# Kernel tuning notes

Hardware: AMD Instinct MI355X
Metric: run time of the kernel (lower is better)

Reference implementation:

```python
import jax, jax.numpy as jnp
import numpy as np

B, S, D = 4, 2048, 1024

def setup_inputs() -> dict:
    key = jax.random.key(0)
    ks = jax.random.split(key, 9)
    sc = 1.0 / np.sqrt(D)
    return {
        "x": jax.random.normal(ks[0], (B, S, D), dtype=jnp.float32),
        "Wq": jax.random.normal(ks[1], (D, D), dtype=jnp.float32) * sc,
        "bq": jnp.zeros((D,), dtype=jnp.float32),
        "Wk": jax.random.normal(ks[2], (D, D), dtype=jnp.float32) * sc,
        "bk": jnp.zeros((D,), dtype=jnp.float32),
        "Wv": jax.random.normal(ks[3], (D, D), dtype=jnp.float32) * sc,
        "bv": jnp.zeros((D,), dtype=jnp.float32),
        "Wo": jax.random.normal(ks[4], (D, D), dtype=jnp.float32) * sc,
        "bo": jnp.zeros((D,), dtype=jnp.float32),
    }

def _gaussian_mask(seq_len, dtype):
    # exp(-0.5*((pos - S/2)/(S/4))^2), shape [1,1,S] -> broadcasts over KEY axis
    pos = jnp.arange(seq_len, dtype=dtype)
    center = seq_len / 2
    sigma = seq_len / 4
    m = jnp.exp(-0.5 * ((pos - center) / sigma) ** 2)
    return m[None, None, :]

def reference(x, Wq, bq, Wk, bk, Wv, bv, Wo, bo):
    d = x.shape[-1]
    Q = x @ Wq.T + bq            # [B,S,D]
    K = x @ Wk.T + bk
    V = x @ Wv.T + bv
    scores = jnp.einsum('bqd,bkd->bqk', Q, K) / jnp.sqrt(jnp.asarray(d, x.dtype))
    scores = scores * _gaussian_mask(x.shape[1], x.dtype)
    attn = jax.nn.softmax(scores, axis=-1)
    out = jnp.einsum('bqk,bkd->bqd', attn, V)
    return out @ Wo.T + bo
```

## Files before the change

kernel.cpp:

```cpp
#include <hip/hip_runtime.h>
#include <math.h>

#define SEQ 2048
#define DIM 1024

typedef __attribute__((ext_vector_type(8))) _Float16 half8;
typedef __attribute__((ext_vector_type(4))) float f32x4;

__device__ __forceinline__ unsigned short f2h(float f) {
    union { _Float16 h; unsigned short u; } c; c.h = (_Float16)f;
    return c.u;
}
__device__ __forceinline__ float gmask(int k) {
    float t = ((float)k - 1024.0f) * (1.0f / 512.0f);
    return expf(-0.5f * t * t);
}
__device__ __forceinline__ void glds16(const unsigned short* gp, unsigned short* lp) {
    __builtin_amdgcn_global_load_lds((const __attribute__((address_space(1))) void*)gp,
                                     (__attribute__((address_space(3))) void*)lp, 16, 0, 0);
}

__device__ __forceinline__ void stage64(const unsigned short* __restrict__ g, int ldK,
                                        unsigned short* lds, int wave, int lane) {
    int row = wave * 32 + (lane >> 3);
    int seg = (lane & 7) ^ (lane >> 3);
    const unsigned short* gp = g + (long)row * ldK + seg * 8;
    unsigned short* lp = lds + wave * 2048;
    glds16(gp, lp);
    glds16(gp + 8 * (long)ldK, lp + 512);
    glds16(gp + 16 * (long)ldK, lp + 1024);
    glds16(gp + 24 * (long)ldK, lp + 1536);
}

enum { EPI_QK = 0, EPI_VT = 1, EPI_EXP = 2, EPI_PV = 3, EPI_OUT = 4 };

template <int EPI>
__device__ __forceinline__ void gemm_body(
    const unsigned short* __restrict__ A, const unsigned short* __restrict__ Bm,
    const float* __restrict__ bias,
    float* __restrict__ Cf, unsigned short* __restrict__ Ch,
    int M, int N, int K, float scale, long sA, long sB, long sC)
{
    __shared__ unsigned short As[128 * 64];
    __shared__ unsigned short Bs[128 * 64];

    const int bz = blockIdx.z;
    const int tid = threadIdx.x;
    const int wave = tid >> 6;
    const int lane = tid & 63;
    const int wm = (wave & 1) * 64;
    const int wn = (wave >> 1) * 64;
    const long m0 = (long)blockIdx.y * 128;
    const long n0 = (long)blockIdx.x * 128;
    const int lm = lane & 15;
    const int lk = lane >> 4;

    const unsigned short* pA = A + bz * sA + m0 * K;
    const unsigned short* pB = Bm + bz * sB + n0 * K;

    f32x4 acc[4][4];
#pragma unroll
    for (int i = 0; i < 4; ++i)
#pragma unroll
        for (int j = 0; j < 4; ++j) {
            acc[i][j].x = 0.f; acc[i][j].y = 0.f; acc[i][j].z = 0.f; acc[i][j].w = 0.f;
        }

    int aoff[4][2], boff[4][2];
#pragma unroll
    for (int i = 0; i < 4; ++i)
#pragma unroll
        for (int t = 0; t < 2; ++t) {
            int ar = wm + i * 16 + lm;
            aoff[i][t] = ar * 64 + (((4 * t + lk) ^ (ar & 7)) << 3);
            int br = wn + i * 16 + lm;
            boff[i][t] = br * 64 + (((4 * t + lk) ^ (br & 7)) << 3);
        }

    const int pr = (wave & 1) * 64 + lane;
    const int ph = wave >> 1;
    float psum = 0.f;

    for (int k0 = 0; k0 < K; k0 += 64) {
        stage64(pA + k0, K, As, wave, lane);
        stage64(pB + k0, K, Bs, wave, lane);
        __syncthreads();

        if (EPI == EPI_PV) {
            const unsigned short* rowp = As + pr * 64;
#pragma unroll
            for (int i2 = 0; i2 < 4; ++i2) {
                half8 h = *(const half8*)(rowp + (((2 * i2 + ph) ^ (pr & 7)) << 3));
#pragma unroll
                for (int e = 0; e < 8; ++e) psum += (float)h[e];
            }
        }

#pragma unroll
        for (int t = 0; t < 2; ++t) {
            half8 a[4], b[4];
#pragma unroll
            for (int i = 0; i < 4; ++i) a[i] = *(const half8*)(As + aoff[i][t]);
#pragma unroll
            for (int j = 0; j < 4; ++j) b[j] = *(const half8*)(Bs + boff[j][t]);
#pragma unroll
            for (int i = 0; i < 4; ++i)
#pragma unroll
                for (int j = 0; j < 4; ++j)
                    acc[i][j] = __builtin_amdgcn_mfma_f32_16x16x32_f16(a[i], b[j], acc[i][j], 0, 0, 0);
        }
        __syncthreads();
    }

    float* rsf = (float*)As;
    if (EPI == EPI_PV) {
        rsf[ph * 128 + pr] = psum;
        __syncthreads();
    }

    const long MD = 8388608;
    float* cF = (EPI == EPI_OUT) ? Cf + bz * sC : (float*)nullptr;
    unsigned short* cH = (EPI != EPI_OUT) ? Ch + bz * sC : (unsigned short*)nullptr;

#pragma unroll
    for (int i = 0; i < 4; ++i) {
        long mrow = m0 + wm + i * 16 + lk * 4;
        int lr = wm + i * 16 + lk * 4;
        float inv4[4];
        if (EPI == EPI_PV) {
#pragma unroll
            for (int r = 0; r < 4; ++r)
                inv4[r] = 1.0f / (rsf[lr + r] + rsf[128 + lr + r]);
        }
#pragma unroll
        for (int j = 0; j < 4; ++j) {
            int n = (int)n0 + wn + j * 16 + lm;
            if (EPI == EPI_QK) {
                int sel = n >> 10;
                int n1 = n & 1023;
                float bs = bias[n];
                unsigned short* dst = cH + (long)sel * MD;
#pragma unroll
                for (int r = 0; r < 4; ++r)
                    dst[(mrow + r) * (long)DIM + n1] = f2h(acc[i][j][r] + bs);
            } else if (EPI == EPI_VT) {
                float bs = bias[n];
                long b = mrow >> 11, s = mrow & 2047;
                long idx = 2 * MD + b * (long)DIM * SEQ + (long)n * SEQ + s;
                unsigned long long pk =
                    (unsigned long long)f2h(acc[i][j].x + bs) |
                    ((unsigned long long)f2h(acc[i][j].y + bs) << 16) |
                    ((unsigned long long)f2h(acc[i][j].z + bs) << 32) |
                    ((unsigned long long)f2h(acc[i][j].w + bs) << 48);
                *(unsigned long long*)(cH + idx) = pk;
            } else if (EPI == EPI_EXP) {
                float mult = scale * gmask(n);
#pragma unroll
                for (int r = 0; r < 4; ++r)
                    cH[(mrow + r) * (long)N + n] = f2h(expf(acc[i][j][r] * mult));
            } else if (EPI == EPI_PV) {
#pragma unroll
                for (int r = 0; r < 4; ++r)
                    cH[(mrow + r) * (long)N + n] = f2h(acc[i][j][r] * inv4[r]);
            } else {
                float bs = bias[n];
#pragma unroll
                for (int r = 0; r < 4; ++r)
                    cF[(mrow + r) * (long)N + n] = acc[i][j][r] + bs;
            }
        }
    }
}

__global__ __launch_bounds__(256, 4) void gemm_qk(
    const unsigned short* __restrict__ A, const unsigned short* __restrict__ Bm,
    const float* __restrict__ bias, float* __restrict__ Cf, unsigned short* __restrict__ Ch,
    int M, int N, int K, float scale, long sA, long sB, long sC)
{ gemm_body<EPI_QK>(A, Bm, bias, Cf, Ch, M, N, K, scale, sA, sB, sC); }

__global__ __launch_bounds__(256, 4) void gemm_v(
    const unsigned short* __restrict__ A, const unsigned short* __restrict__ Bm,
    const float* __restrict__ bias, float* __restrict__ Cf, unsigned short* __restrict__ Ch,
    int M, int N, int K, float scale, long sA, long sB, long sC)
{ gemm_body<EPI_VT>(A, Bm, bias, Cf, Ch, M, N, K, scale, sA, sB, sC); }

__global__ __launch_bounds__(256, 4) void gemm_exp(
    const unsigned short* __restrict__ A, const unsigned short* __restrict__ Bm,
    const float* __restrict__ bias, float* __restrict__ Cf, unsigned short* __restrict__ Ch,
    int M, int N, int K, float scale, long sA, long sB, long sC)
{ gemm_body<EPI_EXP>(A, Bm, bias, Cf, Ch, M, N, K, scale, sA, sB, sC); }

__global__ __launch_bounds__(256, 4) void gemm_pv(
    const unsigned short* __restrict__ A, const unsigned short* __restrict__ Bm,
    const float* __restrict__ bias, float* __restrict__ Cf, unsigned short* __restrict__ Ch,
    int M, int N, int K, float scale, long sA, long sB, long sC)
{ gemm_body<EPI_PV>(A, Bm, bias, Cf, Ch, M, N, K, scale, sA, sB, sC); }

__global__ __launch_bounds__(256, 4) void gemm_out(
    const unsigned short* __restrict__ A, const unsigned short* __restrict__ Bm,
    const float* __restrict__ bias, float* __restrict__ Cf, unsigned short* __restrict__ Ch,
    int M, int N, int K, float scale, long sA, long sB, long sC)
{ gemm_body<EPI_OUT>(A, Bm, bias, Cf, Ch, M, N, K, scale, sA, sB, sC); }

__global__ __launch_bounds__(256) void prep(
    const float* __restrict__ x,
    const float* __restrict__ Wq, const float* __restrict__ Wk,
    const float* __restrict__ Wv, const float* __restrict__ Wo,
    const float* __restrict__ b0, const float* __restrict__ b1, const float* __restrict__ b2,
    unsigned short* __restrict__ xh, unsigned short* __restrict__ Wp, float* __restrict__ bqkv)
{
    long gid = (long)blockIdx.x * 256 + threadIdx.x;
    if (gid < 3072) {
        int sel = (int)(gid >> 10);
        const float* s = sel == 0 ? b0 : sel == 1 ? b1 : b2;
        bqkv[gid] = s[gid & 1023];
    }
    const long NX = 8388608 / 4;
    const long NW = 1048576 / 4;
    const long total = NX + 4 * NW;
    for (long i = gid; i < total; i += (long)gridDim.x * 256) {
        const float* src; unsigned short* dst; long off;
        if (i < NX) { src = x; dst = xh; off = i; }
        else {
            long wi = i - NX;
            int sel = (int)(wi >> 18);
            src = sel == 0 ? Wq : sel == 1 ? Wk : sel == 2 ? Wv : Wo;
            dst = Wp + ((long)sel << 20);
            off = wi & (NW - 1);
        }
        float4 v = ((const float4*)src)[off];
        unsigned long long p = (unsigned long long)f2h(v.x) | ((unsigned long long)f2h(v.y) << 16) |
                               ((unsigned long long)f2h(v.z) << 32) | ((unsigned long long)f2h(v.w) << 48);
        ((unsigned long long*)dst)[off] = p;
    }
}

extern "C" void kernel_launch(void* const* d_in, const int* in_sizes, int n_in,
                              void* d_out, int out_size, void* d_ws, size_t ws_size,
                              hipStream_t stream)
{
    const float* x  = (const float*)d_in[0];
    const float* Wq = (const float*)d_in[1];
    const float* bq = (const float*)d_in[2];
    const float* Wk = (const float*)d_in[3];
    const float* bk = (const float*)d_in[4];
    const float* Wv = (const float*)d_in[5];
    const float* bv = (const float*)d_in[6];
    const float* Wo = (const float*)d_in[7];
    const float* bo = (const float*)d_in[8];
    float* out = (float*)d_out;

    const long MD = 4L * SEQ * DIM;
    const long WW = (long)DIM * DIM;
    const long SD = (long)SEQ * DIM, SS = (long)SEQ * SEQ;

    unsigned short* xh   = (unsigned short*)d_ws;
    unsigned short* Wp   = xh + MD;
    unsigned short* Woh  = Wp + 3 * WW;
    float* bqkv          = (float*)(Wp + 4 * WW);
    unsigned short* Qh   = (unsigned short*)(bqkv + 4096);
    unsigned short* VT   = Qh + 2 * MD;
    unsigned short* expS = Qh + 3 * MD;
    unsigned short* O1   = xh;

    dim3 blk(256);
    prep<<<4096, blk, 0, stream>>>(x, Wq, Wk, Wv, Wo, bq, bk, bv, xh, Wp, bqkv);

    gemm_qk<<<dim3(2 * DIM / 128, (4 * SEQ) / 128, 1), blk, 0, stream>>>(
        xh, Wp, bqkv, nullptr, Qh, 4 * SEQ, 2 * DIM, DIM, 1.0f, 0, 0, 0);
    gemm_v<<<dim3(DIM / 128, (4 * SEQ) / 128, 1), blk, 0, stream>>>(
        xh, Wp + 2 * WW, bqkv + 2048, nullptr, Qh, 4 * SEQ, DIM, DIM, 1.0f, 0, 0, 0);
    gemm_exp<<<dim3(SEQ / 128, SEQ / 128, 4), blk, 0, stream>>>(
        Qh, Qh + MD, nullptr, nullptr, expS, SEQ, SEQ, DIM, 0.03125f, SD, SD, SS);
    gemm_pv<<<dim3(DIM / 128, SEQ / 128, 4), blk, 0, stream>>>(
        expS, VT, nullptr, nullptr, O1, SEQ, DIM, SEQ, 1.0f, SS, (long)DIM * SEQ, SD);
    gemm_out<<<dim3(DIM / 128, (4 * SEQ) / 128, 1), blk, 0, stream>>>(
        O1, Woh, bo, out, nullptr, 4 * SEQ, DIM, DIM, 1.0f, 0, 0, 0);
}
```

Baseline: 293.9 us.

## Compute PV row sums with MFMA against ones and remap block indices

In the PV stage, the per-row softmax denominator was accumulated with scalar LDS reads and adds, then reduced through shared memory. It is now computed as an extra MFMA of each A fragment against a vector of ones, so the sum lands in registers aligned with the accumulator rows and the LDS reduction and its barrier go away. Separately, the linear workgroup id is remapped in strides of eight so consecutive blocks are spread across the grid, likely to balance L2 or XCD locality. The ones-MFMA adds 4 extra MFMAs per k-step for every wave of the PV kernel.

```diff
diff --git a/kernel.cpp b/kernel.cpp
--- a/kernel.cpp
+++ b/kernel.cpp
@@ -44,14 +44,21 @@
     __shared__ unsigned short As[128 * 64];
     __shared__ unsigned short Bs[128 * 64];
 
-    const int bz = blockIdx.z;
+    unsigned p = blockIdx.x + gridDim.x * (blockIdx.y + gridDim.y * blockIdx.z);
+    unsigned nwg = gridDim.x * gridDim.y * gridDim.z;
+    unsigned lw = (p & 7) * (nwg >> 3) + (p >> 3);
+    const int bx = lw % gridDim.x;
+    unsigned r1 = lw / gridDim.x;
+    const int by = r1 % gridDim.y;
+    const int bz = r1 / gridDim.y;
+
     const int tid = threadIdx.x;
     const int wave = tid >> 6;
     const int lane = tid & 63;
     const int wm = (wave & 1) * 64;
     const int wn = (wave >> 1) * 64;
-    const long m0 = (long)blockIdx.y * 128;
-    const long n0 = (long)blockIdx.x * 128;
+    const long m0 = (long)by * 128;
+    const long n0 = (long)bx * 128;
     const int lm = lane & 15;
     const int lk = lane >> 4;
 
@@ -65,6 +72,12 @@
         for (int j = 0; j < 4; ++j) {
             acc[i][j].x = 0.f; acc[i][j].y = 0.f; acc[i][j].z = 0.f; acc[i][j].w = 0.f;
         }
+    f32x4 rs[4];
+#pragma unroll
+    for (int i = 0; i < 4; ++i) { rs[i].x = 0.f; rs[i].y = 0.f; rs[i].z = 0.f; rs[i].w = 0.f; }
+    half8 vone;
+#pragma unroll
+    for (int e = 0; e < 8; ++e) vone[e] = (_Float16)1.0f;
 
     int aoff[4][2], boff[4][2];
 #pragma unroll
@@ -77,25 +90,11 @@
             boff[i][t] = br * 64 + (((4 * t + lk) ^ (br & 7)) << 3);
         }
 
-    const int pr = (wave & 1) * 64 + lane;
-    const int ph = wave >> 1;
-    float psum = 0.f;
-
     for (int k0 = 0; k0 < K; k0 += 64) {
         stage64(pA + k0, K, As, wave, lane);
         stage64(pB + k0, K, Bs, wave, lane);
         __syncthreads();
 
-        if (EPI == EPI_PV) {
-            const unsigned short* rowp = As + pr * 64;
-#pragma unroll
-            for (int i2 = 0; i2 < 4; ++i2) {
-                half8 h = *(const half8*)(rowp + (((2 * i2 + ph) ^ (pr & 7)) << 3));
-#pragma unroll
-                for (int e = 0; e < 8; ++e) psum += (float)h[e];
-            }
-        }
-
 #pragma unroll
         for (int t = 0; t < 2; ++t) {
             half8 a[4], b[4];
@@ -108,13 +107,12 @@
 #pragma unroll
                 for (int j = 0; j < 4; ++j)
                     acc[i][j] = __builtin_amdgcn_mfma_f32_16x16x32_f16(a[i], b[j], acc[i][j], 0, 0, 0);
-        }
-        __syncthreads();
-    }
-
-    float* rsf = (float*)As;
-    if (EPI == EPI_PV) {
-        rsf[ph * 128 + pr] = psum;
+            if (EPI == EPI_PV) {
+#pragma unroll
+                for (int i = 0; i < 4; ++i)
+                    rs[i] = __builtin_amdgcn_mfma_f32_16x16x32_f16(a[i], vone, rs[i], 0, 0, 0);
+            }
+        }
         __syncthreads();
     }
 
@@ -125,12 +123,11 @@
 #pragma unroll
     for (int i = 0; i < 4; ++i) {
         long mrow = m0 + wm + i * 16 + lk * 4;
-        int lr = wm + i * 16 + lk * 4;
         float inv4[4];
         if (EPI == EPI_PV) {
 #pragma unroll
             for (int r = 0; r < 4; ++r)
-                inv4[r] = 1.0f / (rsf[lr + r] + rsf[128 + lr + r]);
+                inv4[r] = 1.0f / rs[i][r];
         }
 #pragma unroll
         for (int j = 0; j < 4; ++j) {
```

Measured after the change: 291.9 us. No clear change (-0.7%).
